# Kernel optimization log

Measured on AMD Instinct MI355X. Metric: run time of the kernel, lower is better.

## Reference

```python
import jax, jax.numpy as jnp
import numpy as np

N, M, D = 8192, 8192, 256

def setup_inputs() -> dict:
    key = jax.random.key(0)
    ks = jax.random.split(key, 8)
    s = 1.0 / np.sqrt(D)
    return {
        "x_q": jax.random.normal(ks[0], (N, D), dtype=jnp.float32),
        "x_kv": jax.random.normal(ks[1], (M, D), dtype=jnp.float32),
        "Wq": jax.random.uniform(ks[2], (D, D), minval=-s, maxval=s, dtype=jnp.float32),
        "bq": jax.random.uniform(ks[3], (D,), minval=-s, maxval=s, dtype=jnp.float32),
        "Wk": jax.random.uniform(ks[4], (D, D), minval=-s, maxval=s, dtype=jnp.float32),
        "bk": jax.random.uniform(ks[5], (D,), minval=-s, maxval=s, dtype=jnp.float32),
        "Wv": jax.random.uniform(ks[6], (D, D), minval=-s, maxval=s, dtype=jnp.float32),
        "bv": jax.random.uniform(ks[7], (D,), minval=-s, maxval=s, dtype=jnp.float32),
    }

def reference(x_q, x_kv, Wq, bq, Wk, bk, Wv, bv):
    # Linear layers: y = x @ W^T + b (torch convention: W is [out, in])
    q = x_q @ Wq.T + bq          # [N, D]
    k = x_kv @ Wk.T + bk         # [M, D]
    v = x_kv @ Wv.T + bv         # [M, D]
    scale = jnp.sqrt(jnp.asarray(q.shape[1], q.dtype))
    attn = jnp.einsum('nd,md->nm', q, k) / scale  # [N, M]
    attn = jax.nn.softmax(attn, axis=1)
    return attn @ v              # [N, D]
```

## Files before the change

### kernel.cpp

```cpp
#include <hip/hip_runtime.h>

#define NN 8192
#define MM 8192
#define DD 256
#define NPART 8
#define MPART (MM / NPART)
#define BK 64
#define NT (MPART / BK)
#define QT 32

typedef short bf16x8 __attribute__((ext_vector_type(8)));
typedef short bf16x4 __attribute__((ext_vector_type(4)));
typedef float f32x4 __attribute__((ext_vector_type(4)));
typedef float f32x16 __attribute__((ext_vector_type(16)));
typedef unsigned int u32;
typedef u32 u32x2 __attribute__((ext_vector_type(2)));
typedef u32 u32x4 __attribute__((ext_vector_type(4)));

#define GLL16(src, dst) __builtin_amdgcn_global_load_lds( \
    (__attribute__((address_space(1))) void*)(src), \
    (__attribute__((address_space(3))) void*)(dst), 16, 0, 0)

#define SCALE_C 0.0901684403f

static __device__ __forceinline__ short f2bf(float f) {
    unsigned u = __float_as_uint(f);
    u += 0x7fffu + ((u >> 16) & 1u);
    return (short)(u >> 16);
}

static __device__ __forceinline__ unsigned char f2fp8(float a) {
    u32 r;
    asm("v_cvt_pk_fp8_f32 %0, %1, %1" : "=v"(r) : "v"(a));
    return (unsigned char)(r & 0xFFu);
}

static __device__ __forceinline__ u32 cvtpk(float lo, float hi) {
    u32 r;
    asm("v_cvt_pk_bf16_f32 %0, %1, %2" : "=v"(r) : "v"(lo), "v"(hi));
    return r;
}

__global__ __launch_bounds__(256, 2) void proj_kernel(
    const float* __restrict__ xq, const float* __restrict__ xkv,
    const float* __restrict__ Wq, const float* __restrict__ bq,
    const float* __restrict__ Wk, const float* __restrict__ bk,
    const float* __restrict__ Wv, const float* __restrict__ bv,
    unsigned char* __restrict__ q8, unsigned char* __restrict__ k8,
    short* __restrict__ vp)
{
    __shared__ short Xs[64][264];
    __shared__ short Ws[64][264];

    const int bid = blockIdx.x;
    const int mat = bid >> 9;
    const int t = bid & 511;
    const int rt = t >> 2;
    const int ct = t & 3;
    const float* __restrict__ X = (mat == 0) ? xq : xkv;
    const float* __restrict__ W = (mat == 0) ? Wq : ((mat == 1) ? Wk : Wv);
    const float* __restrict__ bias = (mat == 0) ? bq : ((mat == 1) ? bk : bv);

    const int tid = threadIdx.x;
    const int lane = tid & 63;
    const int wv = tid >> 6;
    const int l15 = lane & 15;
    const int lg = lane >> 4;

    #pragma unroll
    for (int i = 0; i < 16; ++i) {
        int c = i * 256 + tid;
        int row = c >> 6;
        int col4 = (c & 63) << 2;
        f32x4 xv = *reinterpret_cast<const f32x4*>(X + (size_t)(rt * 64 + row) * DD + col4);
        f32x4 wr = *reinterpret_cast<const f32x4*>(W + (size_t)(ct * 64 + row) * DD + col4);
        bf16x4 xb, wb;
        #pragma unroll
        for (int j = 0; j < 4; ++j) { xb[j] = f2bf(xv[j]); wb[j] = f2bf(wr[j]); }
        *reinterpret_cast<bf16x4*>(&Xs[row][col4]) = xb;
        *reinterpret_cast<bf16x4*>(&Ws[row][col4]) = wb;
    }
    __syncthreads();

    f32x4 acc[4];
    #pragma unroll
    for (int f = 0; f < 4; ++f) acc[f] = f32x4{0.f, 0.f, 0.f, 0.f};

    #pragma unroll
    for (int kk = 0; kk < 8; ++kk) {
        bf16x8 a = *reinterpret_cast<const bf16x8*>(&Xs[wv * 16 + l15][kk * 32 + lg * 8]);
        #pragma unroll
        for (int f = 0; f < 4; ++f) {
            bf16x8 b = *reinterpret_cast<const bf16x8*>(&Ws[f * 16 + l15][kk * 32 + lg * 8]);
            acc[f] = __builtin_amdgcn_mfma_f32_16x16x32_bf16(a, b, acc[f], 0, 0, 0);
        }
    }

    #pragma unroll
    for (int f = 0; f < 4; ++f) {
        const int o = ct * 64 + f * 16 + l15;
        const float bsv = bias[o];
        if (mat == 2) {
            bf16x4 pk;
            #pragma unroll
            for (int r = 0; r < 4; ++r) pk[r] = f2bf(acc[f][r] + bsv);
            const int mb = rt * 64 + wv * 16 + lg * 4;
            *reinterpret_cast<bf16x4*>(&vp[(size_t)(mb >> 6) * 16384 + o * 64 + (mb & 63)]) = pk;
        } else if (mat == 0) {
            #pragma unroll
            for (int r = 0; r < 4; ++r) {
                const int rowg = rt * 64 + wv * 16 + lg * 4 + r;
                q8[(size_t)rowg * DD + o] = f2fp8(acc[f][r] + bsv);
            }
        } else {
            #pragma unroll
            for (int r = 0; r < 4; ++r) {
                const int rowg = rt * 64 + wv * 16 + lg * 4 + r;
                k8[(size_t)(o >> 3) * (MM * 8) + (size_t)rowg * 8 + (o & 7)] = f2fp8(acc[f][r] + bsv);
            }
        }
    }
}

__global__ __launch_bounds__(512, 2) void attn_kernel(
    const unsigned char* __restrict__ qg, const unsigned char* __restrict__ kg,
    const short* __restrict__ vp, float* __restrict__ outpT,
    float* __restrict__ statm, float* __restrict__ statl)
{
    extern __shared__ short lds[];
    short* KsBase = lds;
    short* VsBase = lds + 3 * 8192;

    const int bid = blockIdx.x;
    const int p = bid & 7;
    const int qt = bid >> 3;
    const int q0 = qt * 256;
    const int tile0 = p * NT;

    const int tid = threadIdx.x;
    const int lane = tid & 63;
    const int w = tid >> 6;
    const int l31 = lane & 31;
    const int h = lane >> 5;

    long qf8[16];
    {
        const unsigned char* qr = qg + (size_t)(q0 + w * 32 + l31) * DD + h * 8;
        #pragma unroll
        for (int kt = 0; kt < 16; ++kt)
            qf8[kt] = __builtin_bit_cast(long, *reinterpret_cast<const u32x2*>(qr + kt * 16));
    }

    int koff[2], jdstK[2], voff[4], jdstV[4];
    #pragma unroll
    for (int i = 0; i < 2; ++i) {
        const int j = w * 2 + i;
        const int pl = 2 * j + (lane >> 5);
        koff[i] = pl * (MM * 8) + (lane & 31) * 16;
        jdstK[i] = __builtin_amdgcn_readfirstlane(j * 512);
    }
    #pragma unroll
    for (int i = 0; i < 4; ++i) {
        const int j = w * 4 + i;
        const int d = j * 8 + (lane >> 3);
        const int cl = ((lane & 7) - (d & 7)) & 7;
        voff[i] = d * 64 + (cl << 3);
        jdstV[i] = __builtin_amdgcn_readfirstlane(j * 512);
    }

    f32x16 o[8];
    #pragma unroll
    for (int dt = 0; dt < 8; ++dt)
        #pragma unroll
        for (int i = 0; i < 16; ++i) o[dt][i] = 0.f;
    float mrun = -1e30f, lrun = 0.f;

    #pragma unroll
    for (int i = 0; i < 2; ++i)
        GLL16(kg + (size_t)tile0 * 512 + koff[i], KsBase + jdstK[i]);
    #pragma unroll
    for (int i = 0; i < 4; ++i)
        GLL16(vp + (size_t)tile0 * 16384 + voff[i], VsBase + jdstV[i]);
    #pragma unroll
    for (int i = 0; i < 2; ++i)
        GLL16(kg + (size_t)(tile0 + 1) * 512 + koff[i], KsBase + 8192 + jdstK[i]);
    asm volatile("s_waitcnt vmcnt(2)\n\ts_barrier" ::: "memory");

    int kR = 0, kN = 1, kW = 2;
    #pragma unroll 1
    for (int t = 0; t < NT; ++t) {
        const char* kb = (const char*)(KsBase + kR * 8192);
        const char* vb = (const char*)(VsBase + (t & 1) * 16384);

        if (t + 1 < NT) {
            const size_t tb = (size_t)(tile0 + t + 1) * 16384;
            short* vd = VsBase + ((t + 1) & 1) * 16384;
            #pragma unroll
            for (int i = 0; i < 4; ++i) GLL16(vp + tb + voff[i], vd + jdstV[i]);
        }
        if (t + 2 < NT) {
            const size_t tb = (size_t)(tile0 + t + 2) * 512;
            short* kd = KsBase + kW * 8192;
            #pragma unroll
            for (int i = 0; i < 2; ++i) GLL16(kg + tb + koff[i], kd + jdstK[i]);
        }

        f32x16 sL, sH;
        #pragma unroll
        for (int i = 0; i < 16; ++i) { sL[i] = 0.f; sH[i] = 0.f; }
        __builtin_amdgcn_s_setprio(1);
        #pragma unroll
        for (int kt = 0; kt < 16; ++kt) {
            const int gb = (kt * 2 + h) * 512 + l31 * 8;
            long aL = __builtin_bit_cast(long, *reinterpret_cast<const u32x2*>(kb + gb));
            long aH = __builtin_bit_cast(long, *reinterpret_cast<const u32x2*>(kb + gb + 256));
            sL = __builtin_amdgcn_mfma_f32_32x32x16_fp8_fp8(aL, qf8[kt], sL, 0, 0, 0);
            sH = __builtin_amdgcn_mfma_f32_32x32x16_fp8_fp8(aH, qf8[kt], sH, 0, 0, 0);
        }
        __builtin_amdgcn_s_setprio(0);
        #pragma unroll
        for (int i = 0; i < 16; ++i) { sL[i] *= SCALE_C; sH[i] *= SCALE_C; }

        float mx;
        {
            float a0 = fmaxf(fmaxf(sL[0], sL[1]), fmaxf(sL[2], sL[3]));
            float a1 = fmaxf(fmaxf(sL[4], sL[5]), fmaxf(sL[6], sL[7]));
            float a2 = fmaxf(fmaxf(sL[8], sL[9]), fmaxf(sL[10], sL[11]));
            float a3 = fmaxf(fmaxf(sL[12], sL[13]), fmaxf(sL[14], sL[15]));
            float b0 = fmaxf(fmaxf(sH[0], sH[1]), fmaxf(sH[2], sH[3]));
            float b1 = fmaxf(fmaxf(sH[4], sH[5]), fmaxf(sH[6], sH[7]));
            float b2 = fmaxf(fmaxf(sH[8], sH[9]), fmaxf(sH[10], sH[11]));
            float b3 = fmaxf(fmaxf(sH[12], sH[13]), fmaxf(sH[14], sH[15]));
            mx = fmaxf(fmaxf(fmaxf(a0, a1), fmaxf(a2, a3)),
                       fmaxf(fmaxf(b0, b1), fmaxf(b2, b3)));
            mx = fmaxf(mx, __shfl_xor(mx, 32));
        }
        if (__any(mx > mrun + 11.5f)) {
            const float mn = fmaxf(mrun, mx);
            const float al = __builtin_amdgcn_exp2f(mrun - mn);
            mrun = mn;
            lrun *= al;
            #pragma unroll
            for (int dt = 0; dt < 8; ++dt)
                #pragma unroll
                for (int i = 0; i < 16; ++i) o[dt][i] *= al;
        }
        #pragma unroll
        for (int i = 0; i < 16; ++i) {
            sL[i] = __builtin_amdgcn_exp2f(sL[i] - mrun);
            sH[i] = __builtin_amdgcn_exp2f(sH[i] - mrun);
        }
        {
            float r0 = ((sL[0] + sL[1]) + (sL[2] + sL[3])) + ((sL[4] + sL[5]) + (sL[6] + sL[7]));
            float r1 = ((sL[8] + sL[9]) + (sL[10] + sL[11])) + ((sL[12] + sL[13]) + (sL[14] + sL[15]));
            float r2 = ((sH[0] + sH[1]) + (sH[2] + sH[3])) + ((sH[4] + sH[5]) + (sH[6] + sH[7]));
            float r3 = ((sH[8] + sH[9]) + (sH[10] + sH[11])) + ((sH[12] + sH[13]) + (sH[14] + sH[15]));
            float rs = (r0 + r1) + (r2 + r3);
            rs += __shfl_xor(rs, 32);
            lrun += rs;
        }

        bf16x8 pb[4];
        #pragma unroll
        for (int half = 0; half < 2; ++half) {
            const f32x16& sv = half ? sH : sL;
            #pragma unroll
            for (int g = 0; g < 2; ++g) {
                u32 pa = cvtpk(sv[g * 8 + 0], sv[g * 8 + 1]);
                u32 pbq = cvtpk(sv[g * 8 + 2], sv[g * 8 + 3]);
                u32 pc = cvtpk(sv[g * 8 + 4], sv[g * 8 + 5]);
                u32 pd = cvtpk(sv[g * 8 + 6], sv[g * 8 + 7]);
                const u32 xa = (u32)__shfl_xor((int)pa, 32);
                const u32 xb = (u32)__shfl_xor((int)pbq, 32);
                const u32 xc = (u32)__shfl_xor((int)pc, 32);
                const u32 xd = (u32)__shfl_xor((int)pd, 32);
                u32x4 bb;
                bb[0] = h ? xc : pa;
                bb[1] = h ? xd : pbq;
                bb[2] = h ? pc : xa;
                bb[3] = h ? pd : xb;
                pb[half * 2 + g] = __builtin_bit_cast(bf16x8, bb);
            }
        }

        __builtin_amdgcn_s_setprio(1);
        #pragma unroll
        for (int dt = 0; dt < 8; ++dt) {
            const int d = dt * 32 + l31;
            const char* rbase = vb + d * 128;
            const int rot = d & 7;
            bf16x8 a0 = *reinterpret_cast<const bf16x8*>(rbase + (((0 + h + rot) & 7) << 4));
            bf16x8 a1 = *reinterpret_cast<const bf16x8*>(rbase + (((2 + h + rot) & 7) << 4));
            bf16x8 a2 = *reinterpret_cast<const bf16x8*>(rbase + (((4 + h + rot) & 7) << 4));
            bf16x8 a3 = *reinterpret_cast<const bf16x8*>(rbase + (((6 + h + rot) & 7) << 4));
            o[dt] = __builtin_amdgcn_mfma_f32_32x32x16_bf16(a0, pb[0], o[dt], 0, 0, 0);
            o[dt] = __builtin_amdgcn_mfma_f32_32x32x16_bf16(a1, pb[1], o[dt], 0, 0, 0);
            o[dt] = __builtin_amdgcn_mfma_f32_32x32x16_bf16(a2, pb[2], o[dt], 0, 0, 0);
            o[dt] = __builtin_amdgcn_mfma_f32_32x32x16_bf16(a3, pb[3], o[dt], 0, 0, 0);
        }
        __builtin_amdgcn_s_setprio(0);

        if (t + 2 < NT) {
            asm volatile("s_waitcnt vmcnt(2)\n\ts_barrier" ::: "memory");
        } else if (t + 1 < NT) {
            asm volatile("s_waitcnt vmcnt(0)\n\ts_barrier" ::: "memory");
        }
        const int tmp = kR; kR = kN; kN = kW; kW = tmp;
    }

    #pragma unroll
    for (int dt = 0; dt < 8; ++dt) {
        #pragma unroll
        for (int i = 0; i < 16; ++i) {
            const int dg = dt * 32 + (i & 3) + 8 * (i >> 2) + 4 * h;
            outpT[((size_t)p * DD + dg) * NN + q0 + w * 32 + l31] = o[dt][i];
        }
    }
    if (h == 0) {
        statm[(size_t)p * NN + q0 + w * 32 + l31] = mrun;
        statl[(size_t)p * NN + q0 + w * 32 + l31] = lrun;
    }
}

__global__ __launch_bounds__(256) void combine_kernel(
    const float* __restrict__ outpT, const float* __restrict__ statm,
    const float* __restrict__ statl, float* __restrict__ out)
{
    __shared__ float Wn[NPART][QT];
    __shared__ float Ot[QT][DD + 4];

    const int q0 = blockIdx.x * QT;
    const int tid = threadIdx.x;

    if (tid < QT) {
        const int q = q0 + tid;
        float mv[NPART], lv[NPART];
        float mM = -1e30f;
        #pragma unroll
        for (int p = 0; p < NPART; ++p) {
            mv[p] = statm[(size_t)p * NN + q];
            lv[p] = statl[(size_t)p * NN + q];
            mM = fmaxf(mM, mv[p]);
        }
        float L = 0.f;
        float wg[NPART];
        #pragma unroll
        for (int p = 0; p < NPART; ++p) {
            wg[p] = exp2f(mv[p] - mM);
            L += wg[p] * lv[p];
        }
        const float inv = 1.0f / L;
        #pragma unroll
        for (int p = 0; p < NPART; ++p) Wn[p][tid] = wg[p] * inv;
    }
    __syncthreads();

    {
        const int q = tid & 31;
        const int ds = tid >> 5;
        #pragma unroll 4
        for (int d = ds; d < DD; d += 8) {
            float acc = 0.f;
            #pragma unroll
            for (int p = 0; p < NPART; ++p)
                acc += Wn[p][q] * outpT[((size_t)p * DD + d) * NN + q0 + q];
            Ot[q][d] = acc;
        }
    }
    __syncthreads();

    {
        const int qq = tid >> 3;
        const int c = tid & 7;
        #pragma unroll
        for (int j = 0; j < 8; ++j) {
            const int d = c * 32 + j * 4;
            *reinterpret_cast<f32x4*>(&out[(size_t)(q0 + qq) * DD + d]) =
                *reinterpret_cast<const f32x4*>(&Ot[qq][d]);
        }
    }
}

extern "C" void kernel_launch(void* const* d_in, const int* in_sizes, int n_in,
                              void* d_out, int out_size, void* d_ws, size_t ws_size,
                              hipStream_t stream) {
    const float* xq  = (const float*)d_in[0];
    const float* xkv = (const float*)d_in[1];
    const float* Wq  = (const float*)d_in[2];
    const float* bq  = (const float*)d_in[3];
    const float* Wk  = (const float*)d_in[4];
    const float* bk  = (const float*)d_in[5];
    const float* Wv  = (const float*)d_in[6];
    const float* bv  = (const float*)d_in[7];
    float* out = (float*)d_out;

    char* ws = (char*)d_ws;
    unsigned char* qb8 = (unsigned char*)(ws);
    unsigned char* kb8 = (unsigned char*)(ws + ((size_t)4 << 20));
    short* vpb = (short*)(ws + ((size_t)8 << 20));
    float* outpT = (float*)(ws + ((size_t)12 << 20));
    float* sm = (float*)(ws + ((size_t)12 << 20) + (size_t)NPART * NN * DD * 4);
    float* sl = sm + (size_t)NPART * NN;

    hipFuncSetAttribute(reinterpret_cast<const void*>(attn_kernel),
                        hipFuncAttributeMaxDynamicSharedMemorySize, 114688);

    proj_kernel<<<1536, 256, 0, stream>>>(xq, xkv, Wq, bq, Wk, bk, Wv, bv, qb8, kb8, vpb);
    attn_kernel<<<256, 512, 114688, stream>>>(qb8, kb8, vpb, outpT, sm, sl);
    combine_kernel<<<NN / QT, 256, 0, stream>>>(outpT, sm, sl, out);
}
```

Baseline: 107.2 us.

## Share x_kv tile for K and V projections, store partial outputs in bf16, fold scale into exp

The K and V projection blocks are merged so each block loads and converts the x_kv tile once and computes both K and V, cutting the projection grid from 1536 to 1024 blocks. Bf16 conversion now uses the packed hardware instruction. The attention kernel writes its per-partition outputs as bf16 instead of fp32, which halves the partial-output traffic read by the combine kernel, at some cost in precision. The softmax scale is folded into the exp argument as an fma, removing a separate multiply pass, and the rescale threshold and combine weights are adjusted to work on raw scores.

```diff
diff --git a/kernel.cpp b/kernel.cpp
--- a/kernel.cpp
+++ b/kernel.cpp
@@ -9,8 +9,10 @@
 #define NT (MPART / BK)
 #define QT 32
 
+#define SCALE_C 0.0901684403f
+#define RAW_THR 127.5f
+
 typedef short bf16x8 __attribute__((ext_vector_type(8)));
-typedef short bf16x4 __attribute__((ext_vector_type(4)));
 typedef float f32x4 __attribute__((ext_vector_type(4)));
 typedef float f32x16 __attribute__((ext_vector_type(16)));
 typedef unsigned int u32;
@@ -21,14 +23,6 @@
     (__attribute__((address_space(1))) void*)(src), \
     (__attribute__((address_space(3))) void*)(dst), 16, 0, 0)
 
-#define SCALE_C 0.0901684403f
-
-static __device__ __forceinline__ short f2bf(float f) {
-    unsigned u = __float_as_uint(f);
-    u += 0x7fffu + ((u >> 16) & 1u);
-    return (short)(u >> 16);
-}
-
 static __device__ __forceinline__ unsigned char f2fp8(float a) {
     u32 r;
     asm("v_cvt_pk_fp8_f32 %0, %1, %1" : "=v"(r) : "v"(a));
@@ -39,6 +33,10 @@
     u32 r;
     asm("v_cvt_pk_bf16_f32 %0, %1, %2" : "=v"(r) : "v"(lo), "v"(hi));
     return r;
+}
+
+static __device__ __forceinline__ float bf2f(short s) {
+    return __builtin_bit_cast(float, (u32)((unsigned short)s) << 16);
 }
 
 __global__ __launch_bounds__(256, 2) void proj_kernel(
@@ -53,13 +51,12 @@
     __shared__ short Ws[64][264];
 
     const int bid = blockIdx.x;
-    const int mat = bid >> 9;
+    const int iskv = bid >> 9;
     const int t = bid & 511;
     const int rt = t >> 2;
     const int ct = t & 3;
-    const float* __restrict__ X = (mat == 0) ? xq : xkv;
-    const float* __restrict__ W = (mat == 0) ? Wq : ((mat == 1) ? Wk : Wv);
-    const float* __restrict__ bias = (mat == 0) ? bq : ((mat == 1) ? bk : bv);
+    const float* __restrict__ X = iskv ? xkv : xq;
+    const float* __restrict__ W1 = iskv ? Wk : Wq;
 
     const int tid = threadIdx.x;
     const int lane = tid & 63;
@@ -73,12 +70,12 @@
         int row = c >> 6;
         int col4 = (c & 63) << 2;
         f32x4 xv = *reinterpret_cast<const f32x4*>(X + (size_t)(rt * 64 + row) * DD + col4);
-        f32x4 wr = *reinterpret_cast<const f32x4*>(W + (size_t)(ct * 64 + row) * DD + col4);
-        bf16x4 xb, wb;
-        #pragma unroll
-        for (int j = 0; j < 4; ++j) { xb[j] = f2bf(xv[j]); wb[j] = f2bf(wr[j]); }
-        *reinterpret_cast<bf16x4*>(&Xs[row][col4]) = xb;
-        *reinterpret_cast<bf16x4*>(&Ws[row][col4]) = wb;
+        f32x4 wr = *reinterpret_cast<const f32x4*>(W1 + (size_t)(ct * 64 + row) * DD + col4);
+        u32x2 xb, wb;
+        xb[0] = cvtpk(xv[0], xv[1]); xb[1] = cvtpk(xv[2], xv[3]);
+        wb[0] = cvtpk(wr[0], wr[1]); wb[1] = cvtpk(wr[2], wr[3]);
+        *reinterpret_cast<u32x2*>(&Xs[row][col4]) = xb;
+        *reinterpret_cast<u32x2*>(&Ws[row][col4]) = wb;
     }
     __syncthreads();
 
@@ -96,35 +93,70 @@
         }
     }
 
-    #pragma unroll
-    for (int f = 0; f < 4; ++f) {
-        const int o = ct * 64 + f * 16 + l15;
-        const float bsv = bias[o];
-        if (mat == 2) {
-            bf16x4 pk;
-            #pragma unroll
-            for (int r = 0; r < 4; ++r) pk[r] = f2bf(acc[f][r] + bsv);
-            const int mb = rt * 64 + wv * 16 + lg * 4;
-            *reinterpret_cast<bf16x4*>(&vp[(size_t)(mb >> 6) * 16384 + o * 64 + (mb & 63)]) = pk;
-        } else if (mat == 0) {
+    if (!iskv) {
+        #pragma unroll
+        for (int f = 0; f < 4; ++f) {
+            const int o = ct * 64 + f * 16 + l15;
+            const float bsv = bq[o];
             #pragma unroll
             for (int r = 0; r < 4; ++r) {
                 const int rowg = rt * 64 + wv * 16 + lg * 4 + r;
                 q8[(size_t)rowg * DD + o] = f2fp8(acc[f][r] + bsv);
             }
-        } else {
-            #pragma unroll
-            for (int r = 0; r < 4; ++r) {
-                const int rowg = rt * 64 + wv * 16 + lg * 4 + r;
-                k8[(size_t)(o >> 3) * (MM * 8) + (size_t)rowg * 8 + (o & 7)] = f2fp8(acc[f][r] + bsv);
-            }
-        }
+        }
+        return;
+    }
+
+    #pragma unroll
+    for (int f = 0; f < 4; ++f) {
+        const int o = ct * 64 + f * 16 + l15;
+        const float bsv = bk[o];
+        #pragma unroll
+        for (int r = 0; r < 4; ++r) {
+            const int rowg = rt * 64 + wv * 16 + lg * 4 + r;
+            k8[(size_t)(o >> 3) * (MM * 8) + (size_t)rowg * 8 + (o & 7)] = f2fp8(acc[f][r] + bsv);
+        }
+    }
+
+    __syncthreads();
+    #pragma unroll
+    for (int i = 0; i < 16; ++i) {
+        int c = i * 256 + tid;
+        int row = c >> 6;
+        int col4 = (c & 63) << 2;
+        f32x4 wr = *reinterpret_cast<const f32x4*>(Wv + (size_t)(ct * 64 + row) * DD + col4);
+        u32x2 wb;
+        wb[0] = cvtpk(wr[0], wr[1]); wb[1] = cvtpk(wr[2], wr[3]);
+        *reinterpret_cast<u32x2*>(&Ws[row][col4]) = wb;
+    }
+    __syncthreads();
+
+    #pragma unroll
+    for (int f = 0; f < 4; ++f) acc[f] = f32x4{0.f, 0.f, 0.f, 0.f};
+    #pragma unroll
+    for (int kk = 0; kk < 8; ++kk) {
+        bf16x8 a = *reinterpret_cast<const bf16x8*>(&Xs[wv * 16 + l15][kk * 32 + lg * 8]);
+        #pragma unroll
+        for (int f = 0; f < 4; ++f) {
+            bf16x8 b = *reinterpret_cast<const bf16x8*>(&Ws[f * 16 + l15][kk * 32 + lg * 8]);
+            acc[f] = __builtin_amdgcn_mfma_f32_16x16x32_bf16(a, b, acc[f], 0, 0, 0);
+        }
+    }
+    #pragma unroll
+    for (int f = 0; f < 4; ++f) {
+        const int o = ct * 64 + f * 16 + l15;
+        const float bsv = bv[o];
+        const int mb = rt * 64 + wv * 16 + lg * 4;
+        u32 w0 = cvtpk(acc[f][0] + bsv, acc[f][1] + bsv);
+        u32 w1 = cvtpk(acc[f][2] + bsv, acc[f][3] + bsv);
+        u32x2 pk; pk[0] = w0; pk[1] = w1;
+        *reinterpret_cast<u32x2*>(&vp[(size_t)(mb >> 6) * 16384 + o * 64 + (mb & 63)]) = pk;
     }
 }
 
 __global__ __launch_bounds__(512, 2) void attn_kernel(
     const unsigned char* __restrict__ qg, const unsigned char* __restrict__ kg,
-    const short* __restrict__ vp, float* __restrict__ outpT,
+    const short* __restrict__ vp, short* __restrict__ outpB,
     float* __restrict__ statm, float* __restrict__ statl)
 {
     extern __shared__ short lds[];
@@ -218,8 +250,6 @@
             sH = __builtin_amdgcn_mfma_f32_32x32x16_fp8_fp8(aH, qf8[kt], sH, 0, 0, 0);
         }
         __builtin_amdgcn_s_setprio(0);
-        #pragma unroll
-        for (int i = 0; i < 16; ++i) { sL[i] *= SCALE_C; sH[i] *= SCALE_C; }
 
         float mx;
         {
@@ -235,9 +265,9 @@
                        fmaxf(fmaxf(b0, b1), fmaxf(b2, b3)));
             mx = fmaxf(mx, __shfl_xor(mx, 32));
         }
-        if (__any(mx > mrun + 11.5f)) {
+        if (__any(mx > mrun + RAW_THR)) {
             const float mn = fmaxf(mrun, mx);
-            const float al = __builtin_amdgcn_exp2f(mrun - mn);
+            const float al = __builtin_amdgcn_exp2f((mrun - mn) * SCALE_C);
             mrun = mn;
             lrun *= al;
             #pragma unroll
@@ -245,10 +275,11 @@
                 #pragma unroll
                 for (int i = 0; i < 16; ++i) o[dt][i] *= al;
         }
+        const float msc = -mrun * SCALE_C;
         #pragma unroll
         for (int i = 0; i < 16; ++i) {
-            sL[i] = __builtin_amdgcn_exp2f(sL[i] - mrun);
-            sH[i] = __builtin_amdgcn_exp2f(sH[i] - mrun);
+            sL[i] = __builtin_amdgcn_exp2f(fmaf(sL[i], SCALE_C, msc));
+            sH[i] = __builtin_amdgcn_exp2f(fmaf(sH[i], SCALE_C, msc));
         }
         {
             float r0 = ((sL[0] + sL[1]) + (sL[2] + sL[3])) + ((sL[4] + sL[5]) + (sL[6] + sL[7]));
@@ -308,22 +339,25 @@
         const int tmp = kR; kR = kN; kN = kW; kW = tmp;
     }
 
+    const int qc = q0 + w * 32 + l31;
     #pragma unroll
     for (int dt = 0; dt < 8; ++dt) {
         #pragma unroll
-        for (int i = 0; i < 16; ++i) {
+        for (int i = 0; i < 16; i += 2) {
+            const u32 two = cvtpk(o[dt][i], o[dt][i + 1]);
             const int dg = dt * 32 + (i & 3) + 8 * (i >> 2) + 4 * h;
-            outpT[((size_t)p * DD + dg) * NN + q0 + w * 32 + l31] = o[dt][i];
+            outpB[((size_t)p * DD + dg) * NN + qc] = (short)(two & 0xFFFFu);
+            outpB[((size_t)p * DD + dg + 1) * NN + qc] = (short)(two >> 16);
         }
     }
     if (h == 0) {
-        statm[(size_t)p * NN + q0 + w * 32 + l31] = mrun;
-        statl[(size_t)p * NN + q0 + w * 32 + l31] = lrun;
+        statm[(size_t)p * NN + qc] = mrun;
+        statl[(size_t)p * NN + qc] = lrun;
     }
 }
 
 __global__ __launch_bounds__(256) void combine_kernel(
-    const float* __restrict__ outpT, const float* __restrict__ statm,
+    const short* __restrict__ outpB, const float* __restrict__ statm,
     const float* __restrict__ statl, float* __restrict__ out)
 {
     __shared__ float Wn[NPART][QT];
@@ -346,7 +380,7 @@
         float wg[NPART];
         #pragma unroll
         for (int p = 0; p < NPART; ++p) {
-            wg[p] = exp2f(mv[p] - mM);
+            wg[p] = exp2f((mv[p] - mM) * SCALE_C);
             L += wg[p] * lv[p];
         }
         const float inv = 1.0f / L;
@@ -363,7 +397,7 @@
             float acc = 0.f;
             #pragma unroll
             for (int p = 0; p < NPART; ++p)
-                acc += Wn[p][q] * outpT[((size_t)p * DD + d) * NN + q0 + q];
+                acc += Wn[p][q] * bf2f(outpB[((size_t)p * DD + d) * NN + q0 + q]);
             Ot[q][d] = acc;
         }
     }
@@ -398,14 +432,14 @@
     unsigned char* qb8 = (unsigned char*)(ws);
     unsigned char* kb8 = (unsigned char*)(ws + ((size_t)4 << 20));
     short* vpb = (short*)(ws + ((size_t)8 << 20));
-    float* outpT = (float*)(ws + ((size_t)12 << 20));
-    float* sm = (float*)(ws + ((size_t)12 << 20) + (size_t)NPART * NN * DD * 4);
+    short* outpB = (short*)(ws + ((size_t)12 << 20));
+    float* sm = (float*)(ws + ((size_t)12 << 20) + (size_t)NPART * NN * DD * 2);
     float* sl = sm + (size_t)NPART * NN;
 
     hipFuncSetAttribute(reinterpret_cast<const void*>(attn_kernel),
                         hipFuncAttributeMaxDynamicSharedMemorySize, 114688);
 
-    proj_kernel<<<1536, 256, 0, stream>>>(xq, xkv, Wq, bq, Wk, bk, Wv, bv, qb8, kb8, vpb);
-    attn_kernel<<<256, 512, 114688, stream>>>(qb8, kb8, vpb, outpT, sm, sl);
-    combine_kernel<<<NN / QT, 256, 0, stream>>>(outpT, sm, sl, out);
-}
+    proj_kernel<<<1024, 256, 0, stream>>>(xq, xkv, Wq, bq, Wk, bk, Wv, bv, qb8, kb8, vpb);
+    attn_kernel<<<256, 512, 114688, stream>>>(qb8, kb8, vpb, outpB, sm, sl);
+    combine_kernel<<<NN / QT, 256, 0, stream>>>(outpB, sm, sl, out);
+}
```

Result: faster. 101.6 us (-5.2%).
